# Kernel optimization log

Measured on AMD Instinct MI355X. Metric: run time of the kernel, lower is better.

Reference implementation:

```python
import jax, jax.numpy as jnp
import numpy as np

EMBED_DIM = 256
NUM_HEADS = 8
HEAD_DIM = EMBED_DIM // NUM_HEADS
WINDOW = 31
B, S = 4, 2048


def _make_params(key):
    ks = jax.random.split(key, 8)
    sc = 0.05
    Wq = jax.random.normal(ks[0], (NUM_HEADS, EMBED_DIM, HEAD_DIM), jnp.float32) * sc
    bq = jax.random.normal(ks[1], (NUM_HEADS, HEAD_DIM), jnp.float32) * sc
    Wk = jax.random.normal(ks[2], (NUM_HEADS, EMBED_DIM, HEAD_DIM), jnp.float32) * sc
    bk = jax.random.normal(ks[3], (NUM_HEADS, HEAD_DIM), jnp.float32) * sc
    Wv = jax.random.normal(ks[4], (NUM_HEADS, EMBED_DIM, HEAD_DIM), jnp.float32) * sc
    bv = jax.random.normal(ks[5], (NUM_HEADS, HEAD_DIM), jnp.float32) * sc
    Wo = jax.random.normal(ks[6], (NUM_HEADS * HEAD_DIM, EMBED_DIM), jnp.float32) * sc
    bo = jax.random.normal(ks[7], (EMBED_DIM,), jnp.float32) * sc
    return Wq, bq, Wk, bk, Wv, bv, Wo, bo


def setup_inputs() -> dict:
    key = jax.random.key(0)
    k1, k2, k3, k4 = jax.random.split(key, 4)
    eeg = jax.random.normal(k1, (B, S, EMBED_DIM), jnp.float32)
    pps = jax.random.normal(k2, (B, S, EMBED_DIM), jnp.float32)
    e2p = _make_params(k3)
    p2e = _make_params(k4)
    names = ["Wq", "bq", "Wk", "bk", "Wv", "bv", "Wo", "bo"]
    inp = {"eeg": eeg, "pps": pps}
    for n, p in zip(names, e2p):
        inp["e2p_" + n] = p
    for n, p in zip(names, p2e):
        inp["p2e_" + n] = p
    return inp


def _cross_window_attn(q_seq, kv_seq, Wq, bq, Wk, bk, Wv, bv, Wo, bo, window):
    # q_seq, kv_seq: [B, S, D]. Each query position i attends to window of
    # the zero-padded kv sequence centered at i (pad positions get bias-only k/v,
    # matching torch Linear applied to zero vectors).
    b, s, d_in = q_seq.shape
    h, _, hd = Wq.shape
    pad = (window - 1) // 2
    kv_pad = jnp.pad(kv_seq, ((0, 0), (pad, pad), (0, 0)))
    Q = jnp.einsum('bsd,hde->bhse', q_seq, Wq) + bq[None, :, None, :]
    K = jnp.einsum('bsd,hde->bhse', kv_pad, Wk) + bk[None, :, None, :]
    V = jnp.einsum('bsd,hde->bhse', kv_pad, Wv) + bv[None, :, None, :]
    idx = jnp.arange(s)[:, None] + jnp.arange(window)[None, :]  # [S, W]
    Kw = K[:, :, idx, :]  # [B, H, S, W, hd]
    Vw = V[:, :, idx, :]
    scores = jnp.einsum('bhse,bhswe->bhsw', Q, Kw) / np.sqrt(hd).astype(np.float32)
    attn = jax.nn.softmax(scores, axis=-1)
    out = jnp.einsum('bhsw,bhswe->bhse', attn, Vw)  # [B, H, S, hd]
    out = out.transpose(0, 2, 1, 3).reshape(b, s, h * hd)
    return out @ Wo + bo


def reference(eeg, pps,
              e2p_Wq, e2p_bq, e2p_Wk, e2p_bk, e2p_Wv, e2p_bv, e2p_Wo, e2p_bo,
              p2e_Wq, p2e_bq, p2e_Wk, p2e_bk, p2e_Wv, p2e_bv, p2e_Wo, p2e_bo):
    fused_eeg = _cross_window_attn(eeg, pps, e2p_Wq, e2p_bq, e2p_Wk, e2p_bk,
                                   e2p_Wv, e2p_bv, e2p_Wo, e2p_bo, WINDOW)
    fused_pps = _cross_window_attn(pps, eeg, p2e_Wq, p2e_bq, p2e_Wk, p2e_bk,
                                   p2e_Wv, p2e_bv, p2e_Wo, p2e_bo, WINDOW)
    return fused_eeg, fused_pps
```

## Files before the change

kernel.cpp:

```cpp
#include <hip/hip_runtime.h>

static __device__ __forceinline__ float bf2f(unsigned short u) {
    return __uint_as_float(((unsigned int)u) << 16);
}
static __device__ __forceinline__ unsigned short f2bf(float f) {
    unsigned int x = __float_as_uint(f);
    unsigned int lsb = (x >> 16) & 1u;
    x += 0x7fffu + lsb;
    return (unsigned short)(x >> 16);
}

typedef __attribute__((ext_vector_type(8))) short short8;
typedef __attribute__((ext_vector_type(4))) float floatx4;

static __device__ __forceinline__ short8 ldg8(const unsigned short* p) {
    short8 v; __builtin_memcpy(&v, p, 16); return v;
}


__global__ __launch_bounds__(256) void repack_kernel(
    const float* e2p_Wq, const float* e2p_bq,
    const float* e2p_Wk, const float* e2p_bk,
    const float* e2p_Wv, const float* e2p_bv,
    const float* e2p_Wo, const float* e2p_bo,
    const float* p2e_Wq, const float* p2e_bq,
    const float* p2e_Wk, const float* p2e_bk,
    const float* p2e_Wv, const float* p2e_bv,
    const float* p2e_Wo, const float* p2e_bo,
    const float* eeg, const float* pps,
    unsigned short* Wpack, unsigned short* Wopack, float* bias_pack, float* bias2,
    unsigned short* Abf)
{
    __shared__ unsigned short tr[2048];
    const int bid = blockIdx.x, tid = threadIdx.x;

    if (bid < 2048) {
        const int g = bid >> 1, kc_half = (bid & 1) * 4;
        const int inp = g >> 9;
        const int m = (g & 511) * 16 + (tid >> 4);
        const int k8 = kc_half * 4 + (tid & 15);
        const float* src = inp ? pps : eeg;
        float v[8];
        __builtin_memcpy(v, src + (long)m * 256 + k8 * 8, 32);
        unsigned short o[8];
        #pragma unroll
        for (int j = 0; j < 8; ++j) o[j] = f2bf(v[j]);
        const int k8l = tid & 15;
        __builtin_memcpy(&tr[(k8l >> 2) * 512 + ((k8l & 3) * 16 + (tid >> 4)) * 8], o, 16);
        __syncthreads();
        unsigned short t[8];
        __builtin_memcpy(t, &tr[tid * 8], 16);
        __builtin_memcpy(Abf + inp * 2097152 + ((g & 511) * 8 + kc_half) * 512 + tid * 8, t, 16);
        return;
    }
    if (bid < 2240) {
        int idx = (bid - 2048) * 256 + tid;
        int inp = idx / 24576, r = idx % 24576;
        int n = (r & 15) | ((r >> 9) << 4);
        int k8 = (r >> 4) & 31;
        int kc = k8 >> 2, q4 = k8 & 3, kb = k8 * 8;
        int proj = n / 256, h = (n % 256) / 32, e = n % 32;
        const float* W;
        if (inp == 0) W = (proj == 0) ? e2p_Wq : (proj == 1) ? p2e_Wk : p2e_Wv;
        else          W = (proj == 0) ? p2e_Wq : (proj == 1) ? e2p_Wk : e2p_Wv;
        unsigned short o[8];
        #pragma unroll
        for (int j = 0; j < 8; ++j) o[j] = f2bf(W[h * 8192 + (kb + j) * 32 + e]);
        __builtin_memcpy(Wpack + inp * 196608 + ((n >> 4) * 8 + kc) * 512 + (q4 * 16 + (n & 15)) * 8, o, 16);
        return;
    }
    if (bid < 2304) {
        int i2 = (bid - 2240) * 256 + tid;
        int dir = i2 / 8192, r = i2 % 8192;
        int n = (r & 15) | ((r >> 9) << 4);
        int k8 = (r >> 4) & 31;
        int kc = k8 >> 2, q4 = k8 & 3, kb = k8 * 8;
        const float* Wo = dir ? p2e_Wo : e2p_Wo;
        unsigned short o[8];
        #pragma unroll
        for (int j = 0; j < 8; ++j) o[j] = f2bf(Wo[(kb + j) * 256 + n]);
        __builtin_memcpy(Wopack + dir * 65536 + ((n >> 4) * 8 + kc) * 512 + (q4 * 16 + (n & 15)) * 8, o, 16);
        return;
    }
    {
        int idx = (bid - 2304) * 256 + tid;
        if (idx < 1536) {
            int inp = idx / 768, n = idx % 768;
            int proj = n / 256, he = n % 256;
            const float* bsrc;
            if (inp == 0) bsrc = (proj == 0) ? e2p_bq : (proj == 1) ? p2e_bk : p2e_bv;
            else          bsrc = (proj == 0) ? p2e_bq : (proj == 1) ? e2p_bk : e2p_bv;
            bias_pack[idx] = bsrc[he];
        } else {
            int j = idx - 1536;
            int dir = j / 256, n = j % 256;
            bias2[j] = (dir == 0 ? e2p_bo : p2e_bo)[n];
        }
    }
}

__global__ __launch_bounds__(256) void mfma_gemm_kernel(
    const unsigned short* __restrict__ A0, const unsigned short* __restrict__ A1,
    const unsigned short* __restrict__ B0f, const unsigned short* __restrict__ B1f,
    const float* __restrict__ bias0, const float* __restrict__ bias1,
    unsigned short* __restrict__ C0, unsigned short* __restrict__ C1,
    int N)
{
    __shared__ __align__(16) unsigned short Cs[128][136];

    const int z = blockIdx.z;
    const unsigned short* A = z ? A1 : A0;
    const unsigned short* Bf = z ? B1f : B0f;
    const float* bias = z ? bias1 : bias0;
    unsigned short* C = z ? C1 : C0;

    const int tid = threadIdx.x;
    const long m0 = (long)blockIdx.x * 128;
    const int n0 = blockIdx.y * 128;

    const int lane = tid & 63;
    const int wv = tid >> 6;
    const int wm = (wv >> 1) * 64, wn = (wv & 1) * 64;
    const int fr = lane & 15, q4 = lane >> 4;

    const unsigned short* Aw = A + ((blockIdx.x * 8 + (wm >> 4)) * 8) * 512 + lane * 8;
    const unsigned short* Bw = Bf + ((blockIdx.y * 8 + (wn >> 4)) * 8) * 512 + lane * 8;

    floatx4 acc[4][4] = {};
    short8 af[2][4], bf_[2][4];

    #pragma unroll
    for (int i = 0; i < 4; ++i) af[0][i] = ldg8(Aw + i * 4096);
    #pragma unroll
    for (int j = 0; j < 4; ++j) bf_[0][j] = ldg8(Bw + j * 4096);

    #pragma unroll
    for (int kc = 0; kc < 8; ++kc) {
        const int cur = kc & 1, nxt = cur ^ 1;
        if (kc < 7) {
            #pragma unroll
            for (int i = 0; i < 4; ++i) af[nxt][i] = ldg8(Aw + (i * 8 + kc + 1) * 512);
            #pragma unroll
            for (int j = 0; j < 4; ++j) bf_[nxt][j] = ldg8(Bw + (j * 8 + kc + 1) * 512);
        }
        #pragma unroll
        for (int i = 0; i < 4; ++i)
            #pragma unroll
            for (int j = 0; j < 4; ++j)
                acc[i][j] = __builtin_amdgcn_mfma_f32_16x16x32_bf16(af[cur][i], bf_[cur][j], acc[i][j], 0, 0, 0);
    }

    float bj[4];
    #pragma unroll
    for (int j = 0; j < 4; ++j) bj[j] = bias[n0 + wn + j * 16 + fr];

    const int cr0 = wm + (q4 << 2);
    #pragma unroll
    for (int i = 0; i < 4; ++i)
        #pragma unroll
        for (int j = 0; j < 4; ++j)
            #pragma unroll
            for (int r = 0; r < 4; ++r)
                Cs[cr0 + i * 16 + r][wn + j * 16 + fr] = f2bf(acc[i][j][r] + bj[j]);
    __syncthreads();

    const int rr = tid >> 4, cc = (tid & 15) * 8;
    #pragma unroll
    for (int p = 0; p < 8; ++p) {
        int r = p * 16 + rr;
        unsigned short tmp[8];
        __builtin_memcpy(tmp, &Cs[r][cc], 16);
        __builtin_memcpy(C + (m0 + r) * N + n0 + cc, tmp, 16);
    }
}

#define KVSTR 264
#define PSTR 72
__global__ __launch_bounds__(512, 4) void attn_out_kernel(
    const unsigned short* __restrict__ Y, const float* __restrict__ bias_pack,
    const unsigned short* __restrict__ Wopack, const float* __restrict__ bias2,
    float* __restrict__ out)
{
    __shared__ __align__(16) unsigned short smem[18432 + 16896];
    unsigned short* Ks = smem;
    unsigned short* Vs = smem + 18432;
    unsigned short (*Ps)[32][PSTR] = (unsigned short(*)[32][PSTR])smem;
    unsigned short (*As)[KVSTR] = (unsigned short(*)[KVSTR])(smem + 18432);

    const int s0 = blockIdx.x * 32;
    const int b = blockIdx.y, dir = blockIdx.z;
    const int kvinp = 1 - dir;
    const int tid = threadIdx.x;

    const float* bkv = bias_pack + kvinp * 768;
    const long kvbase = ((long)kvinp * 8192 + b * 2048) * 768;

    {
        const int r = tid >> 3, seg = (tid & 7) * 32;
        const int p = s0 - 15 + r;
        unsigned short tmp[32];
        if (p >= 0 && p < 2048) {
            __builtin_memcpy(tmp, Y + kvbase + (long)p * 768 + 256 + seg, 64);
        } else {
            #pragma unroll
            for (int j = 0; j < 32; ++j) tmp[j] = f2bf(bkv[256 + seg + j]);
        }
        __builtin_memcpy(&Ks[r * KVSTR + seg], tmp, 64);
        if (p >= 0 && p < 2048) {
            __builtin_memcpy(tmp, Y + kvbase + (long)p * 768 + 512 + seg, 64);
        } else {
            #pragma unroll
            for (int j = 0; j < 32; ++j) tmp[j] = f2bf(bkv[512 + seg + j]);
        }
        __builtin_memcpy(&Vs[r * KVSTR + seg], tmp, 64);
    }

    const int lane = tid & 63;
    const int wv = tid >> 6;
    const int fr = lane & 15, q4 = lane >> 4;
    short8 aq[2];
    #pragma unroll
    for (int it = 0; it < 2; ++it)
        aq[it] = ldg8(Y + ((long)dir * 8192 + b * 2048 + s0 + it * 16 + fr) * 768 + wv * 32 + q4 * 8);

    __syncthreads();

    floatx4 sacc[2][3] = {};
    #pragma unroll
    for (int kvt = 0; kvt < 4; ++kvt) {
        short8 bk_ = *(const short8*)&Ks[(kvt * 16 + fr) * KVSTR + wv * 32 + q4 * 8];
        if (kvt < 3) sacc[0][kvt]     = __builtin_amdgcn_mfma_f32_16x16x32_bf16(aq[0], bk_, sacc[0][kvt], 0, 0, 0);
        if (kvt > 0) sacc[1][kvt - 1] = __builtin_amdgcn_mfma_f32_16x16x32_bf16(aq[1], bk_, sacc[1][kvt - 1], 0, 0, 0);
    }

    float sv[2][3][4];
    float rs[2][4];
    #pragma unroll
    for (int it = 0; it < 2; ++it) {
        float mx[4] = {-3.0e38f, -3.0e38f, -3.0e38f, -3.0e38f};
        #pragma unroll
        for (int kt = 0; kt < 3; ++kt)
            #pragma unroll
            for (int reg = 0; reg < 4; ++reg) {
                int i = it * 16 + q4 * 4 + reg;
                int jc = (it + kt) * 16 + fr;
                int d = jc - i;
                float x = (d >= 0 && d <= 30) ? sacc[it][kt][reg] * 0.17677669529663687f : -3.0e38f;
                sv[it][kt][reg] = x;
                mx[reg] = fmaxf(mx[reg], x);
            }
        #pragma unroll
        for (int off = 1; off < 16; off <<= 1)
            #pragma unroll
            for (int reg = 0; reg < 4; ++reg)
                mx[reg] = fmaxf(mx[reg], __shfl_xor(mx[reg], off));
        float ps[4] = {};
        #pragma unroll
        for (int kt = 0; kt < 3; ++kt)
            #pragma unroll
            for (int reg = 0; reg < 4; ++reg) {
                float e = __expf(sv[it][kt][reg] - mx[reg]);
                sv[it][kt][reg] = e;
                ps[reg] += e;
            }
        #pragma unroll
        for (int off = 1; off < 16; off <<= 1)
            #pragma unroll
            for (int reg = 0; reg < 4; ++reg)
                ps[reg] += __shfl_xor(ps[reg], off);
        #pragma unroll
        for (int reg = 0; reg < 4; ++reg) rs[it][reg] = 1.0f / ps[reg];
    }

    __syncthreads();

    #pragma unroll
    for (int it = 0; it < 2; ++it)
        #pragma unroll
        for (int reg = 0; reg < 4; ++reg) {
            int i = it * 16 + q4 * 4 + reg;
            #pragma unroll
            for (int kt = 0; kt < 3; ++kt)
                Ps[wv][i][(it + kt) * 16 + fr] = f2bf(sv[it][kt][reg]);
            Ps[wv][i][(it == 0 ? 48 : 0) + fr] = 0;
        }

    floatx4 oacc[2][2] = {};
    #pragma unroll
    for (int ch = 0; ch < 2; ++ch) {
        short8 ap0 = *(const short8*)&Ps[wv][fr][ch * 32 + q4 * 8];
        short8 ap1 = *(const short8*)&Ps[wv][16 + fr][ch * 32 + q4 * 8];
        #pragma unroll
        for (int et = 0; et < 2; ++et) {
            short8 bv;
            #pragma unroll
            for (int j = 0; j < 8; ++j)
                bv[j] = (short)Vs[(ch * 32 + q4 * 8 + j) * KVSTR + wv * 32 + et * 16 + fr];
            oacc[0][et] = __builtin_amdgcn_mfma_f32_16x16x32_bf16(ap0, bv, oacc[0][et], 0, 0, 0);
            oacc[1][et] = __builtin_amdgcn_mfma_f32_16x16x32_bf16(ap1, bv, oacc[1][et], 0, 0, 0);
        }
    }

    #pragma unroll
    for (int it = 0; it < 2; ++it)
        #pragma unroll
        for (int et = 0; et < 2; ++et)
            #pragma unroll
            for (int reg = 0; reg < 4; ++reg)
                As[it * 16 + q4 * 4 + reg][wv * 32 + et * 16 + fr] = f2bf(oacc[it][et][reg] * rs[it][reg]);

    __syncthreads();

    const unsigned short* Wo = Wopack + dir * 65536 + lane * 8;
    const int nw = wv * 32;
    floatx4 oa[2][2] = {};
    #pragma unroll
    for (int kc = 0; kc < 8; ++kc) {
        short8 ap0 = *(const short8*)&As[fr][kc * 32 + q4 * 8];
        short8 ap1 = *(const short8*)&As[16 + fr][kc * 32 + q4 * 8];
        #pragma unroll
        for (int j = 0; j < 2; ++j) {
            short8 bw = ldg8(Wo + ((wv * 2 + j) * 8 + kc) * 512);
            oa[0][j] = __builtin_amdgcn_mfma_f32_16x16x32_bf16(ap0, bw, oa[0][j], 0, 0, 0);
            oa[1][j] = __builtin_amdgcn_mfma_f32_16x16x32_bf16(ap1, bw, oa[1][j], 0, 0, 0);
        }
    }

    float bj[2];
    #pragma unroll
    for (int j = 0; j < 2; ++j) bj[j] = bias2[dir * 256 + nw + j * 16 + fr];

    float* obase = out + (long)dir * 2097152 + ((long)b * 2048 + s0) * 256;
    #pragma unroll
    for (int it = 0; it < 2; ++it)
        #pragma unroll
        for (int j = 0; j < 2; ++j)
            #pragma unroll
            for (int reg = 0; reg < 4; ++reg)
                obase[(it * 16 + q4 * 4 + reg) * 256 + nw + j * 16 + fr] = oa[it][j][reg] + bj[j];
}

extern "C" void kernel_launch(void* const* d_in, const int* in_sizes, int n_in,
                              void* d_out, int out_size, void* d_ws, size_t ws_size,
                              hipStream_t stream)
{
    float* out = (float*)d_out;

    char* ws = (char*)d_ws;
    unsigned short* Wpack   = (unsigned short*)(ws + 0);
    unsigned short* Wopack  = (unsigned short*)(ws + 786432);
    float*          biasP   = (float*)(ws + 1048576);
    float*          bias2   = (float*)(ws + 1054720);
    unsigned short* Y       = (unsigned short*)(ws + 1056768);
    unsigned short* Abf     = (unsigned short*)(ws + 26222592);

    repack_kernel<<<2312, 256, 0, stream>>>(
        (const float*)d_in[2],  (const float*)d_in[3],
        (const float*)d_in[4],  (const float*)d_in[5],
        (const float*)d_in[6],  (const float*)d_in[7],
        (const float*)d_in[8],  (const float*)d_in[9],
        (const float*)d_in[10], (const float*)d_in[11],
        (const float*)d_in[12], (const float*)d_in[13],
        (const float*)d_in[14], (const float*)d_in[15],
        (const float*)d_in[16], (const float*)d_in[17],
        (const float*)d_in[0],  (const float*)d_in[1],
        Wpack, Wopack, biasP, bias2, Abf);

    mfma_gemm_kernel<<<dim3(64, 6, 2), 256, 0, stream>>>(
        Abf, Abf + 2097152, Wpack, Wpack + 196608, biasP, biasP + 768,
        Y, Y + 8192 * 768, 768);

    attn_out_kernel<<<dim3(64, 4, 2), 512, 0, stream>>>(Y, biasP, Wopack, bias2, out);
}
```

Before: 131.8 us.

## Fuse QKV projection into windowed attention kernel, dropping intermediate buffers

```diff
diff --git a/kernel.cpp b/kernel.cpp
--- a/kernel.cpp
+++ b/kernel.cpp
@@ -1,8 +1,5 @@
 #include <hip/hip_runtime.h>
 
-static __device__ __forceinline__ float bf2f(unsigned short u) {
-    return __uint_as_float(((unsigned int)u) << 16);
-}
 static __device__ __forceinline__ unsigned short f2bf(float f) {
     unsigned int x = __float_as_uint(f);
     unsigned int lsb = (x >> 16) & 1u;
@@ -18,7 +15,7 @@
 }
 
 
-__global__ __launch_bounds__(256) void repack_kernel(
+__global__ __launch_bounds__(256) void repack_w(
     const float* e2p_Wq, const float* e2p_bq,
     const float* e2p_Wk, const float* e2p_bk,
     const float* e2p_Wv, const float* e2p_bv,
@@ -27,34 +24,12 @@
     const float* p2e_Wk, const float* p2e_bk,
     const float* p2e_Wv, const float* p2e_bv,
     const float* p2e_Wo, const float* p2e_bo,
-    const float* eeg, const float* pps,
-    unsigned short* Wpack, unsigned short* Wopack, float* bias_pack, float* bias2,
-    unsigned short* Abf)
+    unsigned short* Wpack, unsigned short* Wopack, float* bias_pack, float* bias2)
 {
-    __shared__ unsigned short tr[2048];
     const int bid = blockIdx.x, tid = threadIdx.x;
 
-    if (bid < 2048) {
-        const int g = bid >> 1, kc_half = (bid & 1) * 4;
-        const int inp = g >> 9;
-        const int m = (g & 511) * 16 + (tid >> 4);
-        const int k8 = kc_half * 4 + (tid & 15);
-        const float* src = inp ? pps : eeg;
-        float v[8];
-        __builtin_memcpy(v, src + (long)m * 256 + k8 * 8, 32);
-        unsigned short o[8];
-        #pragma unroll
-        for (int j = 0; j < 8; ++j) o[j] = f2bf(v[j]);
-        const int k8l = tid & 15;
-        __builtin_memcpy(&tr[(k8l >> 2) * 512 + ((k8l & 3) * 16 + (tid >> 4)) * 8], o, 16);
-        __syncthreads();
-        unsigned short t[8];
-        __builtin_memcpy(t, &tr[tid * 8], 16);
-        __builtin_memcpy(Abf + inp * 2097152 + ((g & 511) * 8 + kc_half) * 512 + tid * 8, t, 16);
-        return;
-    }
-    if (bid < 2240) {
-        int idx = (bid - 2048) * 256 + tid;
+    if (bid < 192) {
+        int idx = bid * 256 + tid;
         int inp = idx / 24576, r = idx % 24576;
         int n = (r & 15) | ((r >> 9) << 4);
         int k8 = (r >> 4) & 31;
@@ -69,8 +44,8 @@
         __builtin_memcpy(Wpack + inp * 196608 + ((n >> 4) * 8 + kc) * 512 + (q4 * 16 + (n & 15)) * 8, o, 16);
         return;
     }
-    if (bid < 2304) {
-        int i2 = (bid - 2240) * 256 + tid;
+    if (bid < 256) {
+        int i2 = (bid - 192) * 256 + tid;
         int dir = i2 / 8192, r = i2 % 8192;
         int n = (r & 15) | ((r >> 9) << 4);
         int k8 = (r >> 4) & 31;
@@ -83,7 +58,7 @@
         return;
     }
     {
-        int idx = (bid - 2304) * 256 + tid;
+        int idx = (bid - 256) * 256 + tid;
         if (idx < 1536) {
             int inp = idx / 768, n = idx % 768;
             int proj = n / 256, he = n % 256;
@@ -99,138 +74,137 @@
     }
 }
 
-__global__ __launch_bounds__(256) void mfma_gemm_kernel(
-    const unsigned short* __restrict__ A0, const unsigned short* __restrict__ A1,
-    const unsigned short* __restrict__ B0f, const unsigned short* __restrict__ B1f,
-    const float* __restrict__ bias0, const float* __restrict__ bias1,
-    unsigned short* __restrict__ C0, unsigned short* __restrict__ C1,
-    int N)
-{
-    __shared__ __align__(16) unsigned short Cs[128][136];
-
-    const int z = blockIdx.z;
-    const unsigned short* A = z ? A1 : A0;
-    const unsigned short* Bf = z ? B1f : B0f;
-    const float* bias = z ? bias1 : bias0;
-    unsigned short* C = z ? C1 : C0;
-
-    const int tid = threadIdx.x;
-    const long m0 = (long)blockIdx.x * 128;
-    const int n0 = blockIdx.y * 128;
-
-    const int lane = tid & 63;
-    const int wv = tid >> 6;
-    const int wm = (wv >> 1) * 64, wn = (wv & 1) * 64;
-    const int fr = lane & 15, q4 = lane >> 4;
-
-    const unsigned short* Aw = A + ((blockIdx.x * 8 + (wm >> 4)) * 8) * 512 + lane * 8;
-    const unsigned short* Bw = Bf + ((blockIdx.y * 8 + (wn >> 4)) * 8) * 512 + lane * 8;
-
-    floatx4 acc[4][4] = {};
-    short8 af[2][4], bf_[2][4];
-
-    #pragma unroll
-    for (int i = 0; i < 4; ++i) af[0][i] = ldg8(Aw + i * 4096);
-    #pragma unroll
-    for (int j = 0; j < 4; ++j) bf_[0][j] = ldg8(Bw + j * 4096);
-
-    #pragma unroll
-    for (int kc = 0; kc < 8; ++kc) {
-        const int cur = kc & 1, nxt = cur ^ 1;
-        if (kc < 7) {
-            #pragma unroll
-            for (int i = 0; i < 4; ++i) af[nxt][i] = ldg8(Aw + (i * 8 + kc + 1) * 512);
-            #pragma unroll
-            for (int j = 0; j < 4; ++j) bf_[nxt][j] = ldg8(Bw + (j * 8 + kc + 1) * 512);
-        }
-        #pragma unroll
-        for (int i = 0; i < 4; ++i)
-            #pragma unroll
-            for (int j = 0; j < 4; ++j)
-                acc[i][j] = __builtin_amdgcn_mfma_f32_16x16x32_bf16(af[cur][i], bf_[cur][j], acc[i][j], 0, 0, 0);
-    }
-
-    float bj[4];
-    #pragma unroll
-    for (int j = 0; j < 4; ++j) bj[j] = bias[n0 + wn + j * 16 + fr];
-
-    const int cr0 = wm + (q4 << 2);
-    #pragma unroll
-    for (int i = 0; i < 4; ++i)
-        #pragma unroll
-        for (int j = 0; j < 4; ++j)
-            #pragma unroll
-            for (int r = 0; r < 4; ++r)
-                Cs[cr0 + i * 16 + r][wn + j * 16 + fr] = f2bf(acc[i][j][r] + bj[j]);
-    __syncthreads();
-
-    const int rr = tid >> 4, cc = (tid & 15) * 8;
-    #pragma unroll
-    for (int p = 0; p < 8; ++p) {
-        int r = p * 16 + rr;
-        unsigned short tmp[8];
-        __builtin_memcpy(tmp, &Cs[r][cc], 16);
-        __builtin_memcpy(C + (m0 + r) * N + n0 + cc, tmp, 16);
-    }
-}
-
-#define KVSTR 264
+#define XSTR 264
+#define KSTR 40
 #define PSTR 72
-__global__ __launch_bounds__(512, 4) void attn_out_kernel(
-    const unsigned short* __restrict__ Y, const float* __restrict__ bias_pack,
+#define VTSTR 72
+#define XKV_OFF 8448
+#define SCR_OFF 25344
+#define SCR_SZ 6144
+__global__ __launch_bounds__(512, 2) void fused_attn(
+    const float* __restrict__ eeg, const float* __restrict__ pps,
+    const unsigned short* __restrict__ Wpack, const float* __restrict__ biasP,
     const unsigned short* __restrict__ Wopack, const float* __restrict__ bias2,
     float* __restrict__ out)
 {
-    __shared__ __align__(16) unsigned short smem[18432 + 16896];
-    unsigned short* Ks = smem;
-    unsigned short* Vs = smem + 18432;
-    unsigned short (*Ps)[32][PSTR] = (unsigned short(*)[32][PSTR])smem;
-    unsigned short (*As)[KVSTR] = (unsigned short(*)[KVSTR])(smem + 18432);
+    __shared__ __align__(16) unsigned short smem[74496];
+    unsigned short* Xq  = smem;
+    unsigned short* Xkv = smem + XKV_OFF;
 
     const int s0 = blockIdx.x * 32;
     const int b = blockIdx.y, dir = blockIdx.z;
     const int kvinp = 1 - dir;
     const int tid = threadIdx.x;
-
-    const float* bkv = bias_pack + kvinp * 768;
-    const long kvbase = ((long)kvinp * 8192 + b * 2048) * 768;
+    const int lane = tid & 63;
+    const int wv = tid >> 6;
+    const int fr = lane & 15, q4 = lane >> 4;
+
+    unsigned short* Qw = smem + SCR_OFF + wv * SCR_SZ;
+    unsigned short* Kw = Qw + 1280;
+    unsigned short* Vt = Qw + 3840;
+
+    float bqq[2], bkk[2], bvv[2], bj2[2];
+    #pragma unroll
+    for (int j = 0; j < 2; ++j) {
+        bqq[j] = biasP[dir * 768 + wv * 32 + j * 16 + fr];
+        bkk[j] = biasP[kvinp * 768 + 256 + wv * 32 + j * 16 + fr];
+        bvv[j] = biasP[kvinp * 768 + 512 + wv * 32 + j * 16 + fr];
+        bj2[j] = bias2[dir * 256 + wv * 32 + j * 16 + fr];
+    }
 
     {
         const int r = tid >> 3, seg = (tid & 7) * 32;
         const int p = s0 - 15 + r;
-        unsigned short tmp[32];
+        const float* Xkvsrc = dir ? eeg : pps;
+        unsigned short o[32];
         if (p >= 0 && p < 2048) {
-            __builtin_memcpy(tmp, Y + kvbase + (long)p * 768 + 256 + seg, 64);
+            float v[32];
+            __builtin_memcpy(v, Xkvsrc + ((long)b * 2048 + p) * 256 + seg, 128);
+            #pragma unroll
+            for (int j = 0; j < 32; ++j) o[j] = f2bf(v[j]);
         } else {
             #pragma unroll
-            for (int j = 0; j < 32; ++j) tmp[j] = f2bf(bkv[256 + seg + j]);
-        }
-        __builtin_memcpy(&Ks[r * KVSTR + seg], tmp, 64);
-        if (p >= 0 && p < 2048) {
-            __builtin_memcpy(tmp, Y + kvbase + (long)p * 768 + 512 + seg, 64);
-        } else {
-            #pragma unroll
-            for (int j = 0; j < 32; ++j) tmp[j] = f2bf(bkv[512 + seg + j]);
-        }
-        __builtin_memcpy(&Vs[r * KVSTR + seg], tmp, 64);
-    }
-
-    const int lane = tid & 63;
-    const int wv = tid >> 6;
-    const int fr = lane & 15, q4 = lane >> 4;
-    short8 aq[2];
+            for (int j = 0; j < 32; ++j) o[j] = 0;
+        }
+        __builtin_memcpy(&Xkv[r * XSTR + seg], o, 64);
+        if (tid < 256) {
+            const float* Xqsrc = dir ? pps : eeg;
+            float v[32];
+            __builtin_memcpy(v, Xqsrc + ((long)b * 2048 + s0 + r) * 256 + seg, 128);
+            unsigned short o2[32];
+            #pragma unroll
+            for (int j = 0; j < 32; ++j) o2[j] = f2bf(v[j]);
+            __builtin_memcpy(&Xq[r * XSTR + seg], o2, 64);
+        }
+    }
+    __syncthreads();
+
+    const unsigned short* WB = Wpack + (long)kvinp * 196608 + lane * 8;
+    const unsigned short* WQ = Wpack + (long)dir * 196608 + lane * 8;
+
+    floatx4 qacc[2][2] = {};
+    #pragma unroll
+    for (int kc = 0; kc < 8; ++kc) {
+        short8 a0 = *(const short8*)&Xq[(fr) * XSTR + kc * 32 + q4 * 8];
+        short8 a1 = *(const short8*)&Xq[(16 + fr) * XSTR + kc * 32 + q4 * 8];
+        #pragma unroll
+        for (int j = 0; j < 2; ++j) {
+            short8 bw = ldg8(WQ + ((2 * wv + j) * 8 + kc) * 512);
+            qacc[0][j] = __builtin_amdgcn_mfma_f32_16x16x32_bf16(a0, bw, qacc[0][j], 0, 0, 0);
+            qacc[1][j] = __builtin_amdgcn_mfma_f32_16x16x32_bf16(a1, bw, qacc[1][j], 0, 0, 0);
+        }
+    }
     #pragma unroll
     for (int it = 0; it < 2; ++it)
-        aq[it] = ldg8(Y + ((long)dir * 8192 + b * 2048 + s0 + it * 16 + fr) * 768 + wv * 32 + q4 * 8);
-
-    __syncthreads();
-
+        #pragma unroll
+        for (int j = 0; j < 2; ++j)
+            #pragma unroll
+            for (int reg = 0; reg < 4; ++reg)
+                Qw[(it * 16 + q4 * 4 + reg) * KSTR + j * 16 + fr] = f2bf(qacc[it][j][reg] + bqq[j]);
+
+    floatx4 kacc[4][2] = {}, vacc[4][2] = {};
+    #pragma unroll
+    for (int kc = 0; kc < 8; ++kc) {
+        short8 ax[4];
+        #pragma unroll
+        for (int mi = 0; mi < 4; ++mi)
+            ax[mi] = *(const short8*)&Xkv[(mi * 16 + fr) * XSTR + kc * 32 + q4 * 8];
+        #pragma unroll
+        for (int j = 0; j < 2; ++j) {
+            short8 kb = ldg8(WB + ((16 + 2 * wv + j) * 8 + kc) * 512);
+            short8 vb = ldg8(WB + ((32 + 2 * wv + j) * 8 + kc) * 512);
+            #pragma unroll
+            for (int mi = 0; mi < 4; ++mi) {
+                kacc[mi][j] = __builtin_amdgcn_mfma_f32_16x16x32_bf16(ax[mi], kb, kacc[mi][j], 0, 0, 0);
+                vacc[mi][j] = __builtin_amdgcn_mfma_f32_16x16x32_bf16(ax[mi], vb, vacc[mi][j], 0, 0, 0);
+            }
+        }
+    }
+    #pragma unroll
+    for (int mi = 0; mi < 4; ++mi)
+        #pragma unroll
+        for (int j = 0; j < 2; ++j)
+            #pragma unroll
+            for (int reg = 0; reg < 4; ++reg)
+                Kw[(mi * 16 + q4 * 4 + reg) * KSTR + j * 16 + fr] = f2bf(kacc[mi][j][reg] + bkk[j]);
+    #pragma unroll
+    for (int mi = 0; mi < 4; ++mi)
+        #pragma unroll
+        for (int j = 0; j < 2; ++j) {
+            unsigned short t4[4];
+            #pragma unroll
+            for (int reg = 0; reg < 4; ++reg) t4[reg] = f2bf(vacc[mi][j][reg] + bvv[j]);
+            __builtin_memcpy(&Vt[(j * 16 + fr) * VTSTR + mi * 16 + q4 * 4], t4, 8);
+        }
+
+    short8 aq0 = *(const short8*)&Qw[fr * KSTR + q4 * 8];
+    short8 aq1 = *(const short8*)&Qw[(16 + fr) * KSTR + q4 * 8];
     floatx4 sacc[2][3] = {};
     #pragma unroll
     for (int kvt = 0; kvt < 4; ++kvt) {
-        short8 bk_ = *(const short8*)&Ks[(kvt * 16 + fr) * KVSTR + wv * 32 + q4 * 8];
-        if (kvt < 3) sacc[0][kvt]     = __builtin_amdgcn_mfma_f32_16x16x32_bf16(aq[0], bk_, sacc[0][kvt], 0, 0, 0);
-        if (kvt > 0) sacc[1][kvt - 1] = __builtin_amdgcn_mfma_f32_16x16x32_bf16(aq[1], bk_, sacc[1][kvt - 1], 0, 0, 0);
+        short8 bk_ = *(const short8*)&Kw[(kvt * 16 + fr) * KSTR + q4 * 8];
+        if (kvt < 3) sacc[0][kvt]     = __builtin_amdgcn_mfma_f32_16x16x32_bf16(aq0, bk_, sacc[0][kvt], 0, 0, 0);
+        if (kvt > 0) sacc[1][kvt - 1] = __builtin_amdgcn_mfma_f32_16x16x32_bf16(aq1, bk_, sacc[1][kvt - 1], 0, 0, 0);
     }
 
     float sv[2][3][4];
@@ -272,8 +246,7 @@
         for (int reg = 0; reg < 4; ++reg) rs[it][reg] = 1.0f / ps[reg];
     }
 
-    __syncthreads();
-
+    unsigned short* Pb = Kw;
     #pragma unroll
     for (int it = 0; it < 2; ++it)
         #pragma unroll
@@ -281,26 +254,26 @@
             int i = it * 16 + q4 * 4 + reg;
             #pragma unroll
             for (int kt = 0; kt < 3; ++kt)
-                Ps[wv][i][(it + kt) * 16 + fr] = f2bf(sv[it][kt][reg]);
-            Ps[wv][i][(it == 0 ? 48 : 0) + fr] = 0;
+                Pb[i * PSTR + (it + kt) * 16 + fr] = f2bf(sv[it][kt][reg]);
+            Pb[i * PSTR + (it == 0 ? 48 : 0) + fr] = 0;
         }
 
     floatx4 oacc[2][2] = {};
     #pragma unroll
     for (int ch = 0; ch < 2; ++ch) {
-        short8 ap0 = *(const short8*)&Ps[wv][fr][ch * 32 + q4 * 8];
-        short8 ap1 = *(const short8*)&Ps[wv][16 + fr][ch * 32 + q4 * 8];
+        short8 ap0 = *(const short8*)&Pb[fr * PSTR + ch * 32 + q4 * 8];
+        short8 ap1 = *(const short8*)&Pb[(16 + fr) * PSTR + ch * 32 + q4 * 8];
         #pragma unroll
         for (int et = 0; et < 2; ++et) {
-            short8 bv;
-            #pragma unroll
-            for (int j = 0; j < 8; ++j)
-                bv[j] = (short)Vs[(ch * 32 + q4 * 8 + j) * KVSTR + wv * 32 + et * 16 + fr];
+            short8 bv = *(const short8*)&Vt[(et * 16 + fr) * VTSTR + ch * 32 + q4 * 8];
             oacc[0][et] = __builtin_amdgcn_mfma_f32_16x16x32_bf16(ap0, bv, oacc[0][et], 0, 0, 0);
             oacc[1][et] = __builtin_amdgcn_mfma_f32_16x16x32_bf16(ap1, bv, oacc[1][et], 0, 0, 0);
         }
     }
 
+    __syncthreads();
+
+    unsigned short (*As)[XSTR] = (unsigned short(*)[XSTR])smem;
     #pragma unroll
     for (int it = 0; it < 2; ++it)
         #pragma unroll
@@ -312,7 +285,6 @@
     __syncthreads();
 
     const unsigned short* Wo = Wopack + dir * 65536 + lane * 8;
-    const int nw = wv * 32;
     floatx4 oa[2][2] = {};
     #pragma unroll
     for (int kc = 0; kc < 8; ++kc) {
@@ -326,10 +298,6 @@
         }
     }
 
-    float bj[2];
-    #pragma unroll
-    for (int j = 0; j < 2; ++j) bj[j] = bias2[dir * 256 + nw + j * 16 + fr];
-
     float* obase = out + (long)dir * 2097152 + ((long)b * 2048 + s0) * 256;
     #pragma unroll
     for (int it = 0; it < 2; ++it)
@@ -337,7 +305,7 @@
         for (int j = 0; j < 2; ++j)
             #pragma unroll
             for (int reg = 0; reg < 4; ++reg)
-                obase[(it * 16 + q4 * 4 + reg) * 256 + nw + j * 16 + fr] = oa[it][j][reg] + bj[j];
+                obase[(it * 16 + q4 * 4 + reg) * 256 + wv * 32 + j * 16 + fr] = oa[it][j][reg] + bj2[j];
 }
 
 extern "C" void kernel_launch(void* const* d_in, const int* in_sizes, int n_in,
@@ -351,10 +319,8 @@
     unsigned short* Wopack  = (unsigned short*)(ws + 786432);
     float*          biasP   = (float*)(ws + 1048576);
     float*          bias2   = (float*)(ws + 1054720);
-    unsigned short* Y       = (unsigned short*)(ws + 1056768);
-    unsigned short* Abf     = (unsigned short*)(ws + 26222592);
-
-    repack_kernel<<<2312, 256, 0, stream>>>(
+
+    repack_w<<<264, 256, 0, stream>>>(
         (const float*)d_in[2],  (const float*)d_in[3],
         (const float*)d_in[4],  (const float*)d_in[5],
         (const float*)d_in[6],  (const float*)d_in[7],
@@ -363,12 +329,9 @@
         (const float*)d_in[12], (const float*)d_in[13],
         (const float*)d_in[14], (const float*)d_in[15],
         (const float*)d_in[16], (const float*)d_in[17],
-        (const float*)d_in[0],  (const float*)d_in[1],
-        Wpack, Wopack, biasP, bias2, Abf);
-
-    mfma_gemm_kernel<<<dim3(64, 6, 2), 256, 0, stream>>>(
-        Abf, Abf + 2097152, Wpack, Wpack + 196608, biasP, biasP + 768,
-        Y, Y + 8192 * 768, 768);
-
-    attn_out_kernel<<<dim3(64, 4, 2), 512, 0, stream>>>(Y, biasP, Wopack, bias2, out);
-}
+        Wpack, Wopack, biasP, bias2);
+
+    fused_attn<<<dim3(64, 4, 2), 512, 0, stream>>>(
+        (const float*)d_in[0], (const float*)d_in[1],
+        Wpack, biasP, Wopack, bias2, out);
+}
```

Measured after the change: 129.0 us. 2.1% less time.
